# Kernel optimization log

Hardware: AMD Instinct MI355X
Metric: run time of the kernel (lower is better)

Reference implementation:

```python
import jax, jax.numpy as jnp
import numpy as np

B, N, E = 2, 2048, 1024   # batch, seq_len, embed_dim (= hidden_dim)
H, HD = 16, 64            # num_heads, head_dim


def setup_inputs() -> dict:
    key = jax.random.key(0)
    ks = jax.random.split(key, 6)
    w = lambda k: jax.random.normal(k, (E, E), jnp.float32) * 0.02
    return {
        "x": jax.random.normal(ks[0], (B, N, E), jnp.float32),
        "Wq": w(ks[1]), "bq": jnp.zeros((E,), jnp.float32),
        "Wk": w(ks[2]), "bk": jnp.zeros((E,), jnp.float32),
        "Wv": w(ks[3]), "bv": jnp.zeros((E,), jnp.float32),
        "Wu": w(ks[4]), "bu": jnp.zeros((E,), jnp.float32),
        "Wo": w(ks[5]), "bo": jnp.zeros((E,), jnp.float32),
        "ln_g": jnp.ones((E,), jnp.float32),
        "ln_b": jnp.zeros((E,), jnp.float32),
    }


def reference(x, Wq, bq, Wk, bk, Wv, bv, Wu, bu, Wo, bo, ln_g, ln_b):
    # projections (torch Linear: x @ W.T + b)
    q = x @ Wq.T + bq
    k = x @ Wk.T + bk
    v = jax.nn.silu(x @ Wv.T + bv)   # uv_act = swish
    u = jax.nn.silu(x @ Wu.T + bu)
    # split heads: [B, N, H*HD] -> [B, H, N, HD]
    split = lambda t: t.reshape(B, N, H, HD).transpose(0, 2, 1, 3)
    q, k, v = split(q), split(k), split(v)
    # non-softmax attention: ReLU on scaled energy (no causal mask)
    energy = jnp.einsum("bhnd,bhmd->bhnm", q, k) / jnp.float32(np.sqrt(HD))
    energy = jax.nn.relu(energy)
    out = jnp.einsum("bhnm,bhmd->bhnd", energy, v)
    # merge heads: [B, H, N, HD] -> [B, N, H*HD]
    out = out.transpose(0, 2, 1, 3).reshape(B, N, H * HD)
    # layernorm over hidden_dim
    mu = out.mean(-1, keepdims=True)
    var = out.var(-1, keepdims=True)
    out = (out - mu) * jax.lax.rsqrt(var + 1e-5) * ln_g + ln_b
    # gate and output projection
    out = u * out
    return out @ Wo.T + bo
```

## Files before the change

kernel.cpp:

```cpp
#include <hip/hip_runtime.h>
#include <stdint.h>

typedef unsigned short u16;
typedef __attribute__((ext_vector_type(8))) short short8;
typedef __attribute__((ext_vector_type(4))) short short4v;
typedef __attribute__((ext_vector_type(4))) float floatx4;
typedef __attribute__((ext_vector_type(4))) int intx4;

#define B_ 2
#define N_ 2048
#define E_ 1024
#define H_ 16
#define HD_ 64
#define M_TOT (B_ * N_)

__device__ __forceinline__ float bf2f(u16 h) {
    union { unsigned u; float f; } c; c.u = ((unsigned)h) << 16; return c.f;
}
__device__ __forceinline__ u16 f2bf(float f) {
    union { float f; unsigned u; } c; c.f = f;
    unsigned r = c.u + 0x7FFFu + ((c.u >> 16) & 1u);
    return (u16)(r >> 16);
}
__device__ __forceinline__ float silu_f(float x) { return x / (1.f + __expf(-x)); }

template <typename T> __device__ __forceinline__ void store_out(T* p, float v);
template <> __device__ __forceinline__ void store_out<u16>(u16* p, float v)    { *p = f2bf(v); }
template <> __device__ __forceinline__ void store_out<float>(float* p, float v) { *p = v; }

__device__ __forceinline__ void gll16(const void* g, void* l) {
    __builtin_amdgcn_global_load_lds(
        (const __attribute__((address_space(1))) void*)g,
        (__attribute__((address_space(3))) void*)l,
        16, 0, 0);
}

__device__ __forceinline__ short4v relu_pack(floatx4 s) {
    union { float f; unsigned u; } c0, c1, c2, c3;
    c0.f = fmaxf(s[0], 0.f); c1.f = fmaxf(s[1], 0.f);
    c2.f = fmaxf(s[2], 0.f); c3.f = fmaxf(s[3], 0.f);
    unsigned lo = __builtin_amdgcn_perm(c1.u + 0x8000u, c0.u + 0x8000u, 0x07060302);
    unsigned hi = __builtin_amdgcn_perm(c3.u + 0x8000u, c2.u + 0x8000u, 0x07060302);
    union { unsigned v[2]; short4v s4; } r; r.v[0] = lo; r.v[1] = hi;
    return r.s4;
}

__launch_bounds__(256, 4)
__global__ void cvt6(const float* __restrict__ s0, const float* __restrict__ s1,
                     const float* __restrict__ s2, const float* __restrict__ s3,
                     const float* __restrict__ s4, const float* __restrict__ s5,
                     u16* __restrict__ d0, u16* __restrict__ d1,
                     u16* __restrict__ d2, u16* __restrict__ d3,
                     u16* __restrict__ d4, u16* __restrict__ d5)
{
    const int z = blockIdx.z;
    if (z > 0 && blockIdx.x >= E_ * E_ / 2048) return;
    const float* src = (z == 0) ? s0 : (z == 1) ? s1 : (z == 2) ? s2
                     : (z == 3) ? s3 : (z == 4) ? s4 : s5;
    u16* dst         = (z == 0) ? d0 : (z == 1) ? d1 : (z == 2) ? d2
                     : (z == 3) ? d3 : (z == 4) ? d4 : d5;
    const int i = (blockIdx.x * 256 + threadIdx.x) * 8;
    floatx4 a = *(const floatx4*)(src + i);
    floatx4 b = *(const floatx4*)(src + i + 4);
    union { u16 h[8]; intx4 v; } o;
    o.h[0] = f2bf(a[0]); o.h[1] = f2bf(a[1]); o.h[2] = f2bf(a[2]); o.h[3] = f2bf(a[3]);
    o.h[4] = f2bf(b[0]); o.h[5] = f2bf(b[1]); o.h[6] = f2bf(b[2]); o.h[7] = f2bf(b[3]);
    *(intx4*)(dst + i) = o.v;
}

template <typename OutT>
__launch_bounds__(256, 2)
__global__ void gemm4(const u16* __restrict__ A,
                      const u16* __restrict__ W0, const u16* __restrict__ W1,
                      const u16* __restrict__ W2, const u16* __restrict__ W3,
                      const float* __restrict__ bi0, const float* __restrict__ bi1,
                      const float* __restrict__ bi2, const float* __restrict__ bi3,
                      OutT* __restrict__ O0, OutT* __restrict__ O1,
                      OutT* __restrict__ O2, OutT* __restrict__ O3,
                      int actmask, int scalemask, int K)
{
    __shared__ u16 a_lds[128 * 32];
    __shared__ u16 b_lds[128 * 32];

    const int z = blockIdx.z;
    const u16* W    = (z == 0) ? W0 : (z == 1) ? W1 : (z == 2) ? W2 : W3;
    const float* Bi = (z == 0) ? bi0 : (z == 1) ? bi1 : (z == 2) ? bi2 : bi3;
    OutT* Out       = (z == 0) ? O0 : (z == 1) ? O1 : (z == 2) ? O2 : O3;
    const bool act = (actmask >> z) & 1;
    const float osc = ((scalemask >> z) & 1) ? 0.125f : 1.0f;

    const int t    = threadIdx.x;
    const int wave = t >> 6, lane = t & 63, quad = lane >> 4, l16 = lane & 15;
    const int wm = wave >> 1, wn = wave & 1;
    const int m0 = blockIdx.y * 128;
    const int n0 = blockIdx.x * 128;

    floatx4 acc[4][4];
    const floatx4 fz = {0.f, 0.f, 0.f, 0.f};
    for (int i = 0; i < 4; i++)
        for (int j = 0; j < 4; j++) acc[i][j] = fz;

    const int ar = t >> 2;
    const int ac = (t & 3) * 8;
    const u16* Ag0 = A + (size_t)(m0 + ar) * K + ac;
    const u16* Ag1 = A + (size_t)(m0 + 64 + ar) * K + ac;
    const u16* Bg0 = W + (size_t)(n0 + ar) * K + ac;
    const u16* Bg1 = W + (size_t)(n0 + 64 + ar) * K + ac;
    u16* al0 = a_lds + wave * 512;
    u16* al1 = a_lds + 2048 + wave * 512;
    u16* bl0 = b_lds + wave * 512;
    u16* bl1 = b_lds + 2048 + wave * 512;

    for (int k0 = 0; k0 < K; k0 += 32) {
        __syncthreads();
        gll16(Ag0 + k0, al0);
        gll16(Ag1 + k0, al1);
        gll16(Bg0 + k0, bl0);
        gll16(Bg1 + k0, bl1);
        __syncthreads();

        short8 af[4], bfr[4];
        for (int i = 0; i < 4; i++)
            af[i]  = *(const short8*)&a_lds[(wm * 64 + i * 16 + l16) * 32 + quad * 8];
        for (int j = 0; j < 4; j++)
            bfr[j] = *(const short8*)&b_lds[(wn * 64 + j * 16 + l16) * 32 + quad * 8];
        for (int i = 0; i < 4; i++)
            for (int j = 0; j < 4; j++)
                acc[i][j] = __builtin_amdgcn_mfma_f32_16x16x32_bf16(af[i], bfr[j], acc[i][j], 0, 0, 0);
    }

    float bias_v[4];
    for (int j = 0; j < 4; j++) bias_v[j] = Bi[n0 + wn * 64 + j * 16 + l16];

    for (int i = 0; i < 4; i++) {
        const int row = m0 + wm * 64 + i * 16 + quad * 4;
        for (int j = 0; j < 4; j++) {
            const int col = n0 + wn * 64 + j * 16 + l16;
            for (int r = 0; r < 4; r++) {
                float v = acc[i][j][r] + bias_v[j];
                if (act) v = silu_f(v);
                v *= osc;
                store_out<OutT>(&Out[(size_t)(row + r) * E_ + col], v);
            }
        }
    }
}

#define LK 72
#define LV 72
#define KSPLIT 4
#define KCHUNK (N_ / KSPLIT)

__launch_bounds__(256, 2)
__global__ void attn(const u16* __restrict__ Q, const u16* __restrict__ Kk,
                     const u16* __restrict__ V,
                     u16* __restrict__ P0, u16* __restrict__ P1,
                     u16* __restrict__ P2, u16* __restrict__ P3)
{
    __shared__ u16 k_lds[64 * LK];
    __shared__ u16 v_lds[64 * LV];

    const int bh = blockIdx.y;
    const int b = bh >> 4, h = bh & 15;
    const int z = blockIdx.z;
    u16* __restrict__ Oa = (z == 0) ? P0 : (z == 1) ? P1 : (z == 2) ? P2 : P3;
    const int key_base = z * KCHUNK;

    const int t = threadIdx.x;
    const int wave = t >> 6, lane = t & 63, quad = lane >> 4, l16 = lane & 15;
    const int q0 = blockIdx.x * 256 + wave * 64;
    const size_t base = (size_t)b * N_ * E_ + h * HD_;

    short8 aq[4][2];
    for (int mi = 0; mi < 4; mi++)
        for (int ks = 0; ks < 2; ks++)
            aq[mi][ks] = *(const short8*)(Q + base + (size_t)(q0 + mi * 16 + l16) * E_ + ks * 32 + quad * 8);

    floatx4 o[4][4];
    const floatx4 fz = {0.f, 0.f, 0.f, 0.f};
    for (int mi = 0; mi < 4; mi++)
        for (int nd = 0; nd < 4; nd++) o[mi][nd] = fz;

    const int srow = t >> 2, sseg = (t & 3) * 16;
    const int prow = (srow & 32) + (((srow >> 2) & 1) << 4)
                   + (((srow >> 3) & 3) << 2) + (srow & 3);
    const u16* Ksrc = Kk + base + (size_t)(key_base + srow) * E_ + sseg;
    u16* kdst = &k_lds[prow * LK + sseg];

    const u16* Vsrc = V + base + (size_t)(key_base + srow) * E_ + sseg;

    for (int kt = 0; kt < KCHUNK / 64; kt++) {
        __syncthreads();
        const u16* kg = Ksrc + (size_t)(kt * 64) * E_;
        const u16* vg = Vsrc + (size_t)(kt * 64) * E_;
        intx4 kv0 = *(const intx4*)(kg);
        intx4 kv1 = *(const intx4*)(kg + 8);
        intx4 vv0 = *(const intx4*)(vg);
        intx4 vv1 = *(const intx4*)(vg + 8);
        *(intx4*)(kdst)     = kv0;
        *(intx4*)(kdst + 8) = kv1;
        const u16* v0p = (const u16*)&vv0;
        const u16* v1p = (const u16*)&vv1;
        for (int i = 0; i < 8; i++) {
            v_lds[(sseg + i) * LV + srow]     = v0p[i];
            v_lds[(sseg + 8 + i) * LV + srow] = v1p[i];
        }
        __syncthreads();

        for (int g = 0; g < 2; g++) {
            short8 ka[2][2];
            for (int tp = 0; tp < 2; tp++)
                for (int ks = 0; ks < 2; ks++)
                    ka[tp][ks] = *(const short8*)&k_lds[(g * 32 + tp * 16 + l16) * LK + ks * 32 + quad * 8];
            short8 bv[4];
            for (int nd = 0; nd < 4; nd++)
                bv[nd] = *(const short8*)&v_lds[(nd * 16 + l16) * LV + g * 32 + quad * 8];

            for (int mi = 0; mi < 4; mi++) {
                floatx4 c0 = __builtin_amdgcn_mfma_f32_16x16x32_bf16(ka[0][0], aq[mi][0], fz, 0, 0, 0);
                c0 = __builtin_amdgcn_mfma_f32_16x16x32_bf16(ka[0][1], aq[mi][1], c0, 0, 0, 0);
                floatx4 c1 = __builtin_amdgcn_mfma_f32_16x16x32_bf16(ka[1][0], aq[mi][0], fz, 0, 0, 0);
                c1 = __builtin_amdgcn_mfma_f32_16x16x32_bf16(ka[1][1], aq[mi][1], c1, 0, 0, 0);
                union { short4v h[2]; short8 s8; } sf;
                sf.h[0] = relu_pack(c0);
                sf.h[1] = relu_pack(c1);
                for (int nd = 0; nd < 4; nd++)
                    o[mi][nd] = __builtin_amdgcn_mfma_f32_16x16x32_bf16(sf.s8, bv[nd], o[mi][nd], 0, 0, 0);
            }
        }
    }

    for (int mi = 0; mi < 4; mi++)
        for (int nd = 0; nd < 4; nd++)
            for (int r = 0; r < 4; r++)
                Oa[(size_t)(b * N_ + q0 + mi * 16 + quad * 4 + r) * E_ + h * HD_ + nd * 16 + l16] =
                    f2bf(o[mi][nd][r]);
}

__launch_bounds__(256, 4)
__global__ void ln_gate(const u16* __restrict__ P0, const u16* __restrict__ P1,
                        const u16* __restrict__ P2, const u16* __restrict__ P3,
                        const u16* __restrict__ U,
                        const float* __restrict__ G, const float* __restrict__ Bb,
                        u16* __restrict__ Out)
{
    const int row = blockIdx.x;
    const int t = threadIdx.x;
    const size_t idx = (size_t)row * E_ + t * 4;
    const short4v a0 = *(const short4v*)(P0 + idx);
    const short4v a1 = *(const short4v*)(P1 + idx);
    const short4v a2 = *(const short4v*)(P2 + idx);
    const short4v a3 = *(const short4v*)(P3 + idx);
    floatx4 v;
    for (int i = 0; i < 4; i++)
        v[i] = bf2f((u16)a0[i]) + bf2f((u16)a1[i]) + bf2f((u16)a2[i]) + bf2f((u16)a3[i]);
    float s  = v[0] + v[1] + v[2] + v[3];
    float ss = v[0] * v[0] + v[1] * v[1] + v[2] * v[2] + v[3] * v[3];
    for (int off = 32; off; off >>= 1) {
        s  += __shfl_down(s, off, 64);
        ss += __shfl_down(ss, off, 64);
    }
    __shared__ float red[8];
    const int wave = t >> 6, lane = t & 63;
    if (lane == 0) { red[wave] = s; red[4 + wave] = ss; }
    __syncthreads();
    const float S  = red[0] + red[1] + red[2] + red[3];
    const float SS = red[4] + red[5] + red[6] + red[7];
    const float mu  = S * (1.f / E_);
    const float var = SS * (1.f / E_) - mu * mu;
    const float rstd = rsqrtf(var + 1e-5f);

    short4v outv;
    for (int i = 0; i < 4; i++) {
        const int e = t * 4 + i;
        float y = (v[i] - mu) * rstd * G[e] + Bb[e];
        y *= bf2f(U[idx + i]);
        outv[i] = (short)f2bf(y);
    }
    *(short4v*)(Out + idx) = outv;
}

extern "C" void kernel_launch(void* const* d_in, const int* in_sizes, int n_in,
                              void* d_out, int out_size, void* d_ws, size_t ws_size,
                              hipStream_t stream)
{
    const float* x   = (const float*)d_in[0];
    const float* Wq  = (const float*)d_in[1];
    const float* bq  = (const float*)d_in[2];
    const float* Wk  = (const float*)d_in[3];
    const float* bk  = (const float*)d_in[4];
    const float* Wv  = (const float*)d_in[5];
    const float* bv  = (const float*)d_in[6];
    const float* Wu  = (const float*)d_in[7];
    const float* bu  = (const float*)d_in[8];
    const float* Wo  = (const float*)d_in[9];
    const float* bo  = (const float*)d_in[10];
    const float* lng = (const float*)d_in[11];
    const float* lnb = (const float*)d_in[12];

    char* ws = (char*)d_ws;
    u16*  qw  = (u16*)(ws);
    u16*  kw  = (u16*)(ws + 8388608);
    u16*  vw  = (u16*)(ws + 16777216);
    u16*  uw  = (u16*)(ws + 25165824);
    u16*  p0  = (u16*)(ws + 33554432);
    u16*  p1  = (u16*)(ws + 41943040);
    u16*  xb  = (u16*)(ws + 50331648);
    u16*  wbq = (u16*)(ws + 58720256);
    u16*  wbk = (u16*)(ws + 60817408);
    u16*  wbv = (u16*)(ws + 62914560);
    u16*  wbu = (u16*)(ws + 65011712);
    u16*  wbo = (u16*)(ws + 67108864);
    u16*  gw  = (u16*)(ws);

    float* out = (float*)d_out;
    u16*  p2  = (u16*)d_out;
    u16*  p3  = (u16*)d_out + 4194304;

    const dim3 blk(256, 1, 1);

    cvt6<<<dim3(M_TOT * E_ / 2048, 1, 6), blk, 0, stream>>>(
        x, Wq, Wk, Wv, Wu, Wo, xb, wbq, wbk, wbv, wbu, wbo);
    gemm4<u16><<<dim3(8, 32, 4), blk, 0, stream>>>(xb, wbq, wbk, wbv, wbu,
                                                   bq, bk, bv, bu,
                                                   qw, kw, vw, uw, 0xC, 0x1, E_);
    attn<<<dim3(N_ / 256, B_ * H_, KSPLIT), blk, 0, stream>>>(qw, kw, vw, p0, p1, p2, p3);
    ln_gate<<<dim3(M_TOT, 1, 1), blk, 0, stream>>>(p0, p1, p2, p3, uw, lng, lnb, gw);
    gemm4<float><<<dim3(8, 32, 1), blk, 0, stream>>>(gw, wbo, wbo, wbo, wbo,
                                                     bo, bo, bo, bo,
                                                     out, out, out, out, 0x0, 0x0, E_);
}
```

Baseline: 226.0 us.

## Halve attention key split and add smaller-tile output projection GEMM

Reduces the attention key-split from 4 to 2, so each block covers more keys and only two partial buffers are written and summed in the layernorm kernel. This cuts partial-output traffic, but with 512 blocks instead of 1024 the attention grid has less parallelism. The output projection now uses a dedicated GEMM with 64x128 tiles, giving 512 blocks instead of 256 to fill more CUs. The new GEMM has no double buffering and a short K-step of 32, so synchronisation overhead may be higher.

```diff
diff --git a/kernel.cpp b/kernel.cpp
--- a/kernel.cpp
+++ b/kernel.cpp
@@ -146,16 +146,72 @@
     }
 }
 
+__launch_bounds__(256, 2)
+__global__ void gemm_out(const u16* __restrict__ A, const u16* __restrict__ W,
+                         const float* __restrict__ Bi, float* __restrict__ Out,
+                         int K)
+{
+    __shared__ u16 a_lds[64 * 32];
+    __shared__ u16 b_lds[128 * 32];
+
+    const int t    = threadIdx.x;
+    const int wave = t >> 6, lane = t & 63, quad = lane >> 4, l16 = lane & 15;
+    const int m0 = blockIdx.y * 64;
+    const int n0 = blockIdx.x * 128;
+
+    floatx4 acc[4][2];
+    const floatx4 fz = {0.f, 0.f, 0.f, 0.f};
+    for (int i = 0; i < 4; i++)
+        for (int j = 0; j < 2; j++) acc[i][j] = fz;
+
+    const int ar = t >> 2;
+    const int ac = (t & 3) * 8;
+    const u16* Ag0 = A + (size_t)(m0 + ar) * K + ac;
+    const u16* Bg0 = W + (size_t)(n0 + ar) * K + ac;
+    const u16* Bg1 = W + (size_t)(n0 + 64 + ar) * K + ac;
+    u16* al0 = a_lds + wave * 512;
+    u16* bl0 = b_lds + wave * 512;
+    u16* bl1 = b_lds + 2048 + wave * 512;
+
+    for (int k0 = 0; k0 < K; k0 += 32) {
+        __syncthreads();
+        gll16(Ag0 + k0, al0);
+        gll16(Bg0 + k0, bl0);
+        gll16(Bg1 + k0, bl1);
+        __syncthreads();
+
+        short8 af[4], bfr[2];
+        for (int i = 0; i < 4; i++)
+            af[i]  = *(const short8*)&a_lds[(i * 16 + l16) * 32 + quad * 8];
+        for (int j = 0; j < 2; j++)
+            bfr[j] = *(const short8*)&b_lds[(wave * 32 + j * 16 + l16) * 32 + quad * 8];
+        for (int i = 0; i < 4; i++)
+            for (int j = 0; j < 2; j++)
+                acc[i][j] = __builtin_amdgcn_mfma_f32_16x16x32_bf16(af[i], bfr[j], acc[i][j], 0, 0, 0);
+    }
+
+    float bias_v[2];
+    for (int j = 0; j < 2; j++) bias_v[j] = Bi[n0 + wave * 32 + j * 16 + l16];
+
+    for (int i = 0; i < 4; i++) {
+        const int row = m0 + i * 16 + quad * 4;
+        for (int j = 0; j < 2; j++) {
+            const int col = n0 + wave * 32 + j * 16 + l16;
+            for (int r = 0; r < 4; r++)
+                Out[(size_t)(row + r) * E_ + col] = acc[i][j][r] + bias_v[j];
+        }
+    }
+}
+
 #define LK 72
 #define LV 72
-#define KSPLIT 4
+#define KSPLIT 2
 #define KCHUNK (N_ / KSPLIT)
 
 __launch_bounds__(256, 2)
 __global__ void attn(const u16* __restrict__ Q, const u16* __restrict__ Kk,
                      const u16* __restrict__ V,
-                     u16* __restrict__ P0, u16* __restrict__ P1,
-                     u16* __restrict__ P2, u16* __restrict__ P3)
+                     u16* __restrict__ P0, u16* __restrict__ P1)
 {
     __shared__ u16 k_lds[64 * LK];
     __shared__ u16 v_lds[64 * LV];
@@ -163,7 +219,7 @@
     const int bh = blockIdx.y;
     const int b = bh >> 4, h = bh & 15;
     const int z = blockIdx.z;
-    u16* __restrict__ Oa = (z == 0) ? P0 : (z == 1) ? P1 : (z == 2) ? P2 : P3;
+    u16* __restrict__ Oa = (z == 0) ? P0 : P1;
     const int key_base = z * KCHUNK;
 
     const int t = threadIdx.x;
@@ -239,7 +295,6 @@
 
 __launch_bounds__(256, 4)
 __global__ void ln_gate(const u16* __restrict__ P0, const u16* __restrict__ P1,
-                        const u16* __restrict__ P2, const u16* __restrict__ P3,
                         const u16* __restrict__ U,
                         const float* __restrict__ G, const float* __restrict__ Bb,
                         u16* __restrict__ Out)
@@ -249,11 +304,9 @@
     const size_t idx = (size_t)row * E_ + t * 4;
     const short4v a0 = *(const short4v*)(P0 + idx);
     const short4v a1 = *(const short4v*)(P1 + idx);
-    const short4v a2 = *(const short4v*)(P2 + idx);
-    const short4v a3 = *(const short4v*)(P3 + idx);
     floatx4 v;
     for (int i = 0; i < 4; i++)
-        v[i] = bf2f((u16)a0[i]) + bf2f((u16)a1[i]) + bf2f((u16)a2[i]) + bf2f((u16)a3[i]);
+        v[i] = bf2f((u16)a0[i]) + bf2f((u16)a1[i]);
     float s  = v[0] + v[1] + v[2] + v[3];
     float ss = v[0] * v[0] + v[1] * v[1] + v[2] * v[2] + v[3] * v[3];
     for (int off = 32; off; off >>= 1) {
@@ -314,8 +367,6 @@
     u16*  gw  = (u16*)(ws);
 
     float* out = (float*)d_out;
-    u16*  p2  = (u16*)d_out;
-    u16*  p3  = (u16*)d_out + 4194304;
 
     const dim3 blk(256, 1, 1);
 
@@ -324,9 +375,7 @@
     gemm4<u16><<<dim3(8, 32, 4), blk, 0, stream>>>(xb, wbq, wbk, wbv, wbu,
                                                    bq, bk, bv, bu,
                                                    qw, kw, vw, uw, 0xC, 0x1, E_);
-    attn<<<dim3(N_ / 256, B_ * H_, KSPLIT), blk, 0, stream>>>(qw, kw, vw, p0, p1, p2, p3);
-    ln_gate<<<dim3(M_TOT, 1, 1), blk, 0, stream>>>(p0, p1, p2, p3, uw, lng, lnb, gw);
-    gemm4<float><<<dim3(8, 32, 1), blk, 0, stream>>>(gw, wbo, wbo, wbo, wbo,
-                                                     bo, bo, bo, bo,
-                                                     out, out, out, out, 0x0, 0x0, E_);
-}
+    attn<<<dim3(N_ / 256, B_ * H_, KSPLIT), blk, 0, stream>>>(qw, kw, vw, p0, p1);
+    ln_gate<<<dim3(M_TOT, 1, 1), blk, 0, stream>>>(p0, p1, uw, lng, lnb, gw);
+    gemm_out<<<dim3(E_ / 128, M_TOT / 64, 1), blk, 0, stream>>>(gw, wbo, bo, out, E_);
+}
```

New measurement: 213.0 us. 5.7% less time.
